# Kernel optimization log

Measured on AMD Instinct MI355X. Metric: run time of the kernel, lower is better.

## Reference

```python
import jax, jax.numpy as jnp
import numpy as np


def setup_inputs() -> dict:
    key = jax.random.key(0)
    ks = jax.random.split(key, 9)
    U, H, R, N = 32, 5120, 160, 16
    return {
        "x": jax.random.normal(ks[0], (U, H), jnp.float32),
        "W_delta": jax.random.normal(ks[1], (H, R), jnp.float32) * 0.02,
        "W_dt": jax.random.normal(ks[2], (R, H), jnp.float32) * 0.02,
        "b_dt": jax.random.normal(ks[3], (H,), jnp.float32) * 0.02,
        "W_B": jax.random.normal(ks[4], (H, N), jnp.float32) * 0.02,
        "W_C": jax.random.normal(ks[5], (H, N), jnp.float32) * 0.02,
        "A_log": jax.random.uniform(ks[6], (H, N), jnp.float32),
        "D": jax.random.normal(ks[7], (H,), jnp.float32),
        "h": jax.random.normal(ks[8], (U, H, N), jnp.float32),
    }


def reference(x, W_delta, W_dt, b_dt, W_B, W_C, A_log, D, h):
    # x: (U,H) single-token decode for U users; h: (U,H,N) recurrent state.
    # delta: low-rank projection then dt_proj, softplus
    dt = jax.nn.softplus((x @ W_delta) @ W_dt + b_dt)          # (U,H)
    A = -jnp.exp(A_log)                                        # (H,N)
    abar = jnp.exp(dt[:, :, None] * A[None, :, :])             # (U,H,N)
    B = x @ W_B                                                # (U,N)
    C = x @ W_C                                                # (U,N)
    # state update: h' = abar*h + (dt*B)*x
    h_new = abar * h + dt[:, :, None] * B[:, None, :] * x[:, :, None]  # (U,H,N)
    # output mix: y = C . h' + D*x
    y = jnp.einsum("uhn,un->uh", h_new, C) + x * D[None, :]    # (U,H)
    return y
```

## Files before the change

kernel.cpp:

```cpp
#include <hip/hip_runtime.h>
#include <math.h>

#define UU 32
#define HH 5120
#define RR 160
#define NN 16


#define TMP_WS  0
#define BP_WS   81920
#define CP_WS   90112
#define TMPR_WS 98304
#define BR_WS   103424
#define CR_WS   103936

__device__ __forceinline__ unsigned short f2bf(float f) {
    unsigned int u = __float_as_uint(f);
    u += 0x7fffu + ((u >> 16) & 1u);
    return (unsigned short)(u >> 16);
}
__device__ __forceinline__ float blo(unsigned int v) { return __uint_as_float(v << 16); }
__device__ __forceinline__ float bhi(unsigned int v) { return __uint_as_float(v & 0xffff0000u); }

__global__ __launch_bounds__(256) void proj_kernel(
    const float* __restrict__ x, const float* __restrict__ Wd,
    const float* __restrict__ WB, const float* __restrict__ WC,
    float* __restrict__ ws)
{
    __shared__ float xs[32 * 36];
    __shared__ float wt[32 * 32];

    const int b = blockIdx.x;
    const int t = threadIdx.x;

    if (b < 80) {
        const int s  = b & 15;
        const int rt = b >> 4;
        const int r0 = rt * 32;
        const int u0 = (t >> 5) * 4;
        const int r  = t & 31;
        float acc[4] = {0.f, 0.f, 0.f, 0.f};

        for (int c = 0; c < 10; c++) {
            const int k0 = s * 320 + c * 32;
            if (c) __syncthreads();
            #pragma unroll
            for (int i = 0; i < 4; i++) {
                int idx = t + i * 256;
                int u = idx >> 5, kk = idx & 31;
                xs[kk * 36 + u] = x[u * HH + k0 + kk];
            }
            {
                int kk = t >> 3, c4 = t & 7;
                *(float4*)&wt[kk * 32 + c4 * 4] =
                    *(const float4*)(Wd + (size_t)(k0 + kk) * RR + r0 + c4 * 4);
            }
            __syncthreads();

            #pragma unroll
            for (int kk = 0; kk < 32; kk++) {
                float4 xv = *(const float4*)&xs[kk * 36 + u0];
                float wv = wt[kk * 32 + r];
                acc[0] += xv.x * wv; acc[1] += xv.y * wv;
                acc[2] += xv.z * wv; acc[3] += xv.w * wv;
            }
        }
        #pragma unroll
        for (int i = 0; i < 4; i++)
            ws[TMP_WS + s * 5120 + (u0 + i) * 160 + r0 + r] = acc[i];
    } else {
        const int sb = b - 80;
        const int k0 = sb * 320;
        const int n  = t & 15;
        const int uu = t >> 4;
        const float* xa = x + uu * HH + k0;
        const float* xb = x + (uu + 16) * HH + k0;
        float aB0 = 0.f, aB1 = 0.f, aC0 = 0.f, aC1 = 0.f;
        #pragma unroll 2
        for (int k4 = 0; k4 < 80; k4++) {
            float4 va = *(const float4*)(xa + k4 * 4);
            float4 vb = *(const float4*)(xb + k4 * 4);
            const int kb = (k0 + k4 * 4) * NN + n;
            #define STEP(D, CMP) { \
                float wb = WB[kb + (D) * NN]; \
                float wc = WC[kb + (D) * NN]; \
                aB0 += va.CMP * wb; aB1 += vb.CMP * wb; \
                aC0 += va.CMP * wc; aC1 += vb.CMP * wc; }
            STEP(0, x) STEP(1, y) STEP(2, z) STEP(3, w)
            #undef STEP
        }
        ws[BP_WS + sb * 512 + uu * 16 + n]        = aB0;
        ws[BP_WS + sb * 512 + (uu + 16) * 16 + n] = aB1;
        ws[CP_WS + sb * 512 + uu * 16 + n]        = aC0;
        ws[CP_WS + sb * 512 + (uu + 16) * 16 + n] = aC1;
    }
}

__global__ __launch_bounds__(256) void reduce_kernel(float* __restrict__ ws)
{
    const int b = blockIdx.x;
    const int t = threadIdx.x;
    if (b < 5) {
        const int idx4 = b * 256 + t;
        float sx = 0.f, sy = 0.f, sz = 0.f, sw = 0.f;
        #pragma unroll
        for (int s = 0; s < 16; s++) {
            float4 v = ((const float4*)(ws + TMP_WS + s * 5120))[idx4];
            sx += v.x; sy += v.y; sz += v.z; sw += v.w;
        }
        float4 o; o.x = sx; o.y = sy; o.z = sz; o.w = sw;
        ((float4*)(ws + TMPR_WS))[idx4] = o;
    } else {
        const int base_in  = (t < 128) ? BP_WS : CP_WS;
        const int base_out = (t < 128) ? BR_WS : CR_WS;
        const int idx4 = t & 127;
        float sx = 0.f, sy = 0.f, sz = 0.f, sw = 0.f;
        #pragma unroll
        for (int s = 0; s < 16; s++) {
            float4 v = ((const float4*)(ws + base_in + s * 512))[idx4];
            sx += v.x; sy += v.y; sz += v.z; sw += v.w;
        }
        float4 o; o.x = sx; o.y = sy; o.z = sz; o.w = sw;
        ((float4*)(ws + base_out))[idx4] = o;
    }
}

__device__ __forceinline__ float softplusf(float v) {
    return (v > 20.f) ? v : log1pf(expf(v));
}

__global__ __launch_bounds__(512) void ssm_kernel(
    const float* __restrict__ x, const float* __restrict__ Wdt,
    const float* __restrict__ bdt, const float* __restrict__ Alog,
    const float* __restrict__ Dv, const float* __restrict__ hstate,
    const float* __restrict__ ws, float* __restrict__ y)
{
    __shared__ unsigned short tmp_b[32 * 168];
    __shared__ unsigned short wsl_b[16 * 168];
    __shared__ float Bl[32 * 20];
    __shared__ float Cl[32 * 20];
    __shared__ float an_l[16 * 20];
    __shared__ float xl[32 * 17];
    __shared__ float bdtl[16];
    __shared__ float Dl[16];

    const int t  = threadIdx.x;
    const int h0 = blockIdx.x * 16;
    const int u  = t >> 4;
    const int q  = t & 15;

    const float* hb = hstate + (size_t)(u * HH + h0 + q) * 16;
    float4 hv[4];
    #pragma unroll
    for (int k = 0; k < 4; k++) hv[k] = ((const float4*)hb)[k];

    #pragma unroll
    for (int i = 0; i < 3; i++) {
        int idx4 = t + i * 512;
        if (idx4 < 1280) {
            float4 v = ((const float4*)(ws + TMPR_WS))[idx4];
            int uu = idx4 / 40, r4 = idx4 % 40;
            unsigned int p0 = (unsigned int)f2bf(v.x) | ((unsigned int)f2bf(v.y) << 16);
            unsigned int p1 = (unsigned int)f2bf(v.z) | ((unsigned int)f2bf(v.w) << 16);
            *(uint2*)&tmp_b[uu * 168 + r4 * 4] = make_uint2(p0, p1);
        }
    }
    #pragma unroll
    for (int i = 0; i < 5; i++) {
        int idx = t + i * 512;
        int r = idx >> 4, hh = idx & 15;
        wsl_b[hh * 168 + r] = f2bf(Wdt[r * HH + h0 + hh]);
    }
    {
        int uu = t >> 4, n = t & 15;
        Bl[uu * 20 + n] = ws[BR_WS + t];
        Cl[uu * 20 + n] = ws[CR_WS + t];
        xl[uu * 17 + n] = x[uu * HH + h0 + n];
    }
    if (t < 256) {
        int hh = t >> 4, n = t & 15;
        an_l[hh * 20 + n] = -expf(Alog[(h0 + hh) * 16 + n]);
    }
    if (t < 16) { bdtl[t] = bdt[h0 + t]; Dl[t] = Dv[h0 + t]; }
    __syncthreads();

    const uint4* ta = (const uint4*)&tmp_b[u * 168];
    const uint4* wp = (const uint4*)&wsl_b[q * 168];
    float ae = 0.f, ao = 0.f;
    #pragma unroll
    for (int c = 0; c < 20; c++) {
        uint4 av = ta[c];
        uint4 wv = wp[c];
        #define MAC(X) \
            ae += blo(av.X) * blo(wv.X); ao += bhi(av.X) * bhi(wv.X);
        MAC(x) MAC(y) MAC(z) MAC(w)
        #undef MAC
    }
    const float dt = softplusf(bdtl[q] + (ae + ao));

    const float xv = xl[u * 17 + q];
    const float K  = dt * xv;
    float yv = xv * Dl[q];
    #pragma unroll
    for (int qq = 0; qq < 4; qq++) {
        float4 h4 = hv[qq];
        float4 b4 = *(const float4*)&Bl[u * 20 + qq * 4];
        float4 c4 = *(const float4*)&Cl[u * 20 + qq * 4];
        float4 a4 = *(const float4*)&an_l[q * 20 + qq * 4];
        yv += (expf(dt * a4.x) * h4.x + K * b4.x) * c4.x;
        yv += (expf(dt * a4.y) * h4.y + K * b4.y) * c4.y;
        yv += (expf(dt * a4.z) * h4.z + K * b4.z) * c4.z;
        yv += (expf(dt * a4.w) * h4.w + K * b4.w) * c4.w;
    }
    y[u * HH + h0 + q] = yv;
}

extern "C" void kernel_launch(void* const* d_in, const int* in_sizes, int n_in,
                              void* d_out, int out_size, void* d_ws, size_t ws_size,
                              hipStream_t stream) {
    const float* x    = (const float*)d_in[0];
    const float* Wd   = (const float*)d_in[1];
    const float* Wdt  = (const float*)d_in[2];
    const float* bdt  = (const float*)d_in[3];
    const float* WB   = (const float*)d_in[4];
    const float* WC   = (const float*)d_in[5];
    const float* Alog = (const float*)d_in[6];
    const float* Dv   = (const float*)d_in[7];
    const float* hst  = (const float*)d_in[8];
    float* y  = (float*)d_out;
    float* ws = (float*)d_ws;

    proj_kernel<<<96, 256, 0, stream>>>(x, Wd, WB, WC, ws);
    reduce_kernel<<<6, 256, 0, stream>>>(ws);
    ssm_kernel<<<320, 512, 0, stream>>>(x, Wdt, bdt, Alog, Dv, hst, ws, y);
}
```

Before: 107.4 us.

## Double split-K blocks in projection and stage whole K-slice in shared memory

The projection kernel now splits the hidden dimension into 32 slices of 160 instead of 16 of 320, launching 192 blocks instead of 96 to fill more compute units. Each block loads its whole x and W_delta slice into shared memory once, with a single barrier, replacing the chunked loop that synchronised every 32 rows. The B/C projection blocks now stage W_B and W_C in shared memory before accumulating. The reduce kernel sums 32 partials instead of 16, which doubles workspace traffic and reduction work.

```diff
diff --git a/kernel.cpp b/kernel.cpp
--- a/kernel.cpp
+++ b/kernel.cpp
@@ -8,11 +8,13 @@
 
 
 #define TMP_WS  0
-#define BP_WS   81920
-#define CP_WS   90112
-#define TMPR_WS 98304
-#define BR_WS   103424
-#define CR_WS   103936
+#define BP_WS   163840
+#define CP_WS   180224
+#define TMPR_WS 196608
+#define BR_WS   201728
+#define CR_WS   202240
+
+#define XS_STRIDE 36
 
 __device__ __forceinline__ unsigned short f2bf(float f) {
     unsigned int u = __float_as_uint(f);
@@ -27,67 +29,78 @@
     const float* __restrict__ WB, const float* __restrict__ WC,
     float* __restrict__ ws)
 {
-    __shared__ float xs[32 * 36];
-    __shared__ float wt[32 * 32];
+    __shared__ float smem[160 * XS_STRIDE + 160 * 32];
 
     const int b = blockIdx.x;
     const int t = threadIdx.x;
 
-    if (b < 80) {
-        const int s  = b & 15;
-        const int rt = b >> 4;
+    if (b < 160) {
+        float* xs = smem;
+        float* wt = smem + 160 * XS_STRIDE;
+        const int s  = b & 31;
+        const int rt = b >> 5;
         const int r0 = rt * 32;
+        const int kbase = s * 160;
         const int u0 = (t >> 5) * 4;
         const int r  = t & 31;
+
+        #pragma unroll
+        for (int i = 0; i < 20; i++) {
+            int idx = t + i * 256;
+            int u = idx / 160, kk = idx % 160;
+            xs[kk * XS_STRIDE + u] = x[u * HH + kbase + kk];
+        }
+        #pragma unroll
+        for (int i = 0; i < 5; i++) {
+            int idx4 = t + i * 256;
+            int kk = idx4 >> 3, r4 = idx4 & 7;
+            *(float4*)&wt[kk * 32 + r4 * 4] =
+                *(const float4*)(Wd + (size_t)(kbase + kk) * RR + r0 + r4 * 4);
+        }
+        __syncthreads();
+
         float acc[4] = {0.f, 0.f, 0.f, 0.f};
-
-        for (int c = 0; c < 10; c++) {
-            const int k0 = s * 320 + c * 32;
-            if (c) __syncthreads();
-            #pragma unroll
-            for (int i = 0; i < 4; i++) {
-                int idx = t + i * 256;
-                int u = idx >> 5, kk = idx & 31;
-                xs[kk * 36 + u] = x[u * HH + k0 + kk];
-            }
-            {
-                int kk = t >> 3, c4 = t & 7;
-                *(float4*)&wt[kk * 32 + c4 * 4] =
-                    *(const float4*)(Wd + (size_t)(k0 + kk) * RR + r0 + c4 * 4);
-            }
-            __syncthreads();
-
-            #pragma unroll
-            for (int kk = 0; kk < 32; kk++) {
-                float4 xv = *(const float4*)&xs[kk * 36 + u0];
-                float wv = wt[kk * 32 + r];
-                acc[0] += xv.x * wv; acc[1] += xv.y * wv;
-                acc[2] += xv.z * wv; acc[3] += xv.w * wv;
-            }
+        #pragma unroll 8
+        for (int kk = 0; kk < 160; kk++) {
+            float4 xv = *(const float4*)&xs[kk * XS_STRIDE + u0];
+            float wv = wt[kk * 32 + r];
+            acc[0] += xv.x * wv; acc[1] += xv.y * wv;
+            acc[2] += xv.z * wv; acc[3] += xv.w * wv;
         }
         #pragma unroll
         for (int i = 0; i < 4; i++)
             ws[TMP_WS + s * 5120 + (u0 + i) * 160 + r0 + r] = acc[i];
     } else {
-        const int sb = b - 80;
-        const int k0 = sb * 320;
+        float* wbl = smem;
+        float* wcl = smem + 160 * 16;
+        const int sb = b - 160;
+        const int k0 = sb * 160;
         const int n  = t & 15;
         const int uu = t >> 4;
+
+        #pragma unroll
+        for (int i = 0; i < 3; i++) {
+            int idx4 = t + i * 256;
+            if (idx4 < 640) {
+                ((float4*)wbl)[idx4] = ((const float4*)(WB + (size_t)k0 * NN))[idx4];
+                ((float4*)wcl)[idx4] = ((const float4*)(WC + (size_t)k0 * NN))[idx4];
+            }
+        }
+        __syncthreads();
+
         const float* xa = x + uu * HH + k0;
         const float* xb = x + (uu + 16) * HH + k0;
         float aB0 = 0.f, aB1 = 0.f, aC0 = 0.f, aC1 = 0.f;
-        #pragma unroll 2
-        for (int k4 = 0; k4 < 80; k4++) {
+        #pragma unroll 4
+        for (int k4 = 0; k4 < 40; k4++) {
             float4 va = *(const float4*)(xa + k4 * 4);
             float4 vb = *(const float4*)(xb + k4 * 4);
-            const int kb = (k0 + k4 * 4) * NN + n;
-            #define STEP(D, CMP) { \
-                float wb = WB[kb + (D) * NN]; \
-                float wc = WC[kb + (D) * NN]; \
-                aB0 += va.CMP * wb; aB1 += vb.CMP * wb; \
-                aC0 += va.CMP * wc; aC1 += vb.CMP * wc; }
-            STEP(0, x) STEP(1, y) STEP(2, z) STEP(3, w)
-            #undef STEP
+            const float* wb = &wbl[k4 * 64 + n];
+            const float* wc = &wcl[k4 * 64 + n];
+            aB0 += va.x * wb[0] + va.y * wb[16] + va.z * wb[32] + va.w * wb[48];
+            aB1 += vb.x * wb[0] + vb.y * wb[16] + vb.z * wb[32] + vb.w * wb[48];
+            aC0 += va.x * wc[0] + va.y * wc[16] + va.z * wc[32] + va.w * wc[48];
+            aC1 += vb.x * wc[0] + vb.y * wc[16] + vb.z * wc[32] + vb.w * wc[48];
         }
         ws[BP_WS + sb * 512 + uu * 16 + n]        = aB0;
         ws[BP_WS + sb * 512 + (uu + 16) * 16 + n] = aB1;
@@ -104,7 +117,7 @@
         const int idx4 = b * 256 + t;
         float sx = 0.f, sy = 0.f, sz = 0.f, sw = 0.f;
         #pragma unroll
-        for (int s = 0; s < 16; s++) {
+        for (int s = 0; s < 32; s++) {
             float4 v = ((const float4*)(ws + TMP_WS + s * 5120))[idx4];
             sx += v.x; sy += v.y; sz += v.z; sw += v.w;
         }
@@ -116,7 +129,7 @@
         const int idx4 = t & 127;
         float sx = 0.f, sy = 0.f, sz = 0.f, sw = 0.f;
         #pragma unroll
-        for (int s = 0; s < 16; s++) {
+        for (int s = 0; s < 32; s++) {
             float4 v = ((const float4*)(ws + base_in + s * 512))[idx4];
             sx += v.x; sy += v.y; sz += v.z; sw += v.w;
         }
@@ -230,7 +243,7 @@
     float* y  = (float*)d_out;
     float* ws = (float*)d_ws;
 
-    proj_kernel<<<96, 256, 0, stream>>>(x, Wd, WB, WC, ws);
+    proj_kernel<<<192, 256, 0, stream>>>(x, Wd, WB, WC, ws);
     reduce_kernel<<<6, 256, 0, stream>>>(ws);
     ssm_kernel<<<320, 512, 0, stream>>>(x, Wdt, bdt, Alog, Dv, hst, ws, y);
 }
```

Result: faster. 98.51 us (-8.3%).
